# Optimization experiments

Hardware: AMD Instinct MI355X
Metric: run time of the kernel (lower is better)

## Reference

```python
import jax, jax.numpy as jnp
import numpy as np

B, T, C = 4, 2048, 1024
H, D = 16, 64  # num_heads, head_dim
WINDOW = 256


def setup_inputs() -> dict:
    key = jax.random.key(0)
    k_x, k_qkv, k_proj, k_qb, k_pb = jax.random.split(key, 5)
    x = jax.random.normal(k_x, (B, T, C), dtype=jnp.float32)
    # xavier-uniform-ish init for qkv weight (as in _reset_parameters)
    lim_qkv = float(np.sqrt(6.0 / (C + 3 * C)))
    qkv_w = jax.random.uniform(k_qkv, (3 * C, C), minval=-lim_qkv, maxval=lim_qkv, dtype=jnp.float32)
    qkv_b = jax.random.normal(k_qb, (3 * C,), dtype=jnp.float32) * 0.02
    lim_p = float(np.sqrt(1.0 / C))
    proj_w = jax.random.uniform(k_proj, (C, C), minval=-lim_p, maxval=lim_p, dtype=jnp.float32)
    proj_b = jax.random.normal(k_pb, (C,), dtype=jnp.float32) * 0.02
    # windowed causal mask: attend to j iff j <= i and i - j < WINDOW
    i = jnp.arange(T)[:, None]
    j = jnp.arange(T)[None, :]
    attn_mask = (j <= i) & (i - j < WINDOW)  # [T, T] bool
    return {"x": x, "attn_mask": attn_mask, "qkv_w": qkv_w, "qkv_b": qkv_b,
            "proj_w": proj_w, "proj_b": proj_b}


def reference(x, attn_mask, qkv_w, qkv_b, proj_w, proj_b):
    qkv = (x @ qkv_w.T + qkv_b).reshape(B, T, 3, H, D)
    qkv = jnp.transpose(qkv, (2, 0, 3, 1, 4))
    q, k, v = qkv[0], qkv[1], qkv[2]
    scale = 1.0 / jnp.sqrt(jnp.asarray(D, dtype=q.dtype))
    scores = jnp.einsum('bhqd,bhkd->bhqk', q, k) * scale  # [B,H,T,T]
    neg = jnp.asarray(jnp.finfo(scores.dtype).min, dtype=scores.dtype)
    scores = jnp.where(attn_mask[None, None], scores, neg)
    attn = jax.nn.softmax(scores, axis=-1)
    out = jnp.einsum('bhqk,bhkd->bhqd', attn, v)  # [B,H,T,D]
    out = jnp.transpose(out, (0, 2, 1, 3)).reshape(B, T, C)
    out = out @ proj_w.T + proj_b
    return out
```

## Files before the change

kernel.cpp:

```cpp
#include <hip/hip_runtime.h>

#define BB 4
#define TT 2048
#define CC 1024
#define HH 16
#define DD 64
#define WIN 256

typedef __attribute__((ext_vector_type(8))) short short8;
typedef __attribute__((ext_vector_type(4))) float floatx4;
typedef unsigned short u16;

__device__ __forceinline__ float bf2f(u16 u) {
    union { unsigned int i; float f; } v; v.i = ((unsigned int)u) << 16; return v.f;
}
__device__ __forceinline__ u16 f2bf(float f) {
    union { float f; unsigned int i; } v; v.f = f;
    unsigned int x = v.i;
    x += ((x >> 16) & 1u) + 0x7FFFu;
    return (u16)(x >> 16);
}

__global__ void cvt_f32_bf16(const float* __restrict__ in, u16* __restrict__ out, int n) {
    int i = (blockIdx.x * 256 + threadIdx.x) * 8;
    if (i >= n) return;
    float4 a = *(const float4*)(in + i);
    float4 b = *(const float4*)(in + i + 4);
    u16 o[8] = { f2bf(a.x), f2bf(a.y), f2bf(a.z), f2bf(a.w),
                 f2bf(b.x), f2bf(b.y), f2bf(b.z), f2bf(b.w) };
    *(uint4*)(out + i) = *(const uint4*)o;
}

__global__ __launch_bounds__(256) void gemm_qkv(
    const u16* __restrict__ A, const u16* __restrict__ Bw,
    const float* __restrict__ bias,
    u16* __restrict__ Qb, u16* __restrict__ Kb, u16* __restrict__ Vb)
{
    const int K = CC;
    __shared__ u16 As[128][40];
    __shared__ u16 Bs[128][40];
    const int tid = threadIdx.x;
    const int wave = tid >> 6, lane = tid & 63;
    const int wm = wave >> 1, wn = wave & 1;
    const int quad = lane >> 4, l15 = lane & 15;
    const int bN = blockIdx.x * 128, bM = blockIdx.y * 128;

    floatx4 acc[4][4] = {};

    for (int k0 = 0; k0 < K; k0 += 32) {
        __syncthreads();
#pragma unroll
        for (int it = 0; it < 2; ++it) {
            int slot = tid + it * 256;
            int r = slot >> 2;
            int c8 = (slot & 3) << 3;
            *(uint4*)&As[r][c8] = *(const uint4*)&A[(size_t)(bM + r) * K + k0 + c8];
            *(uint4*)&Bs[r][c8] = *(const uint4*)&Bw[(size_t)(bN + r) * K + k0 + c8];
        }
        __syncthreads();
        short8 af[4], bf[4];
#pragma unroll
        for (int i = 0; i < 4; ++i) {
            af[i] = *(const short8*)&As[wm * 64 + i * 16 + l15][quad * 8];
            bf[i] = *(const short8*)&Bs[wn * 64 + i * 16 + l15][quad * 8];
        }
#pragma unroll
        for (int mi = 0; mi < 4; ++mi)
#pragma unroll
            for (int ni = 0; ni < 4; ++ni)
                acc[mi][ni] = __builtin_amdgcn_mfma_f32_16x16x32_bf16(af[mi], bf[ni], acc[mi][ni], 0, 0, 0);
    }

#pragma unroll
    for (int mi = 0; mi < 4; ++mi)
#pragma unroll
        for (int ni = 0; ni < 4; ++ni) {
            int col = bN + wn * 64 + ni * 16 + l15;
            float bv = bias[col];
            int which = col >> 10, rem = col & 1023;
            int h = rem >> 6, d = rem & 63;
            u16* dst = which == 0 ? Qb : (which == 1 ? Kb : Vb);
#pragma unroll
            for (int rg = 0; rg < 4; ++rg) {
                int row = bM + wm * 64 + mi * 16 + quad * 4 + rg;
                int b = row >> 11, t = row & 2047;
                float v = acc[mi][ni][rg] + bv;
                dst[(((size_t)(b * HH + h)) * TT + t) * DD + d] = f2bf(v);
            }
        }
}

__global__ __launch_bounds__(256) void gemm_proj(
    const u16* __restrict__ A, const u16* __restrict__ Bw,
    const float* __restrict__ bias, float* __restrict__ Out)
{
    const int K = CC;
    __shared__ u16 As[128][40];
    __shared__ u16 Bs[128][40];
    const int tid = threadIdx.x;
    const int wave = tid >> 6, lane = tid & 63;
    const int wm = wave >> 1, wn = wave & 1;
    const int quad = lane >> 4, l15 = lane & 15;
    const int bN = blockIdx.x * 128, bM = blockIdx.y * 128;

    floatx4 acc[4][4] = {};

    for (int k0 = 0; k0 < K; k0 += 32) {
        __syncthreads();
#pragma unroll
        for (int it = 0; it < 2; ++it) {
            int slot = tid + it * 256;
            int r = slot >> 2;
            int c8 = (slot & 3) << 3;
            *(uint4*)&As[r][c8] = *(const uint4*)&A[(size_t)(bM + r) * K + k0 + c8];
            *(uint4*)&Bs[r][c8] = *(const uint4*)&Bw[(size_t)(bN + r) * K + k0 + c8];
        }
        __syncthreads();
        short8 af[4], bf[4];
#pragma unroll
        for (int i = 0; i < 4; ++i) {
            af[i] = *(const short8*)&As[wm * 64 + i * 16 + l15][quad * 8];
            bf[i] = *(const short8*)&Bs[wn * 64 + i * 16 + l15][quad * 8];
        }
#pragma unroll
        for (int mi = 0; mi < 4; ++mi)
#pragma unroll
            for (int ni = 0; ni < 4; ++ni)
                acc[mi][ni] = __builtin_amdgcn_mfma_f32_16x16x32_bf16(af[mi], bf[ni], acc[mi][ni], 0, 0, 0);
    }

#pragma unroll
    for (int mi = 0; mi < 4; ++mi)
#pragma unroll
        for (int ni = 0; ni < 4; ++ni) {
            int col = bN + wn * 64 + ni * 16 + l15;
            float bv = bias[col];
#pragma unroll
            for (int rg = 0; rg < 4; ++rg) {
                int row = bM + wm * 64 + mi * 16 + quad * 4 + rg;
                Out[(size_t)row * CC + col] = acc[mi][ni][rg] + bv;
            }
        }
}

__global__ __launch_bounds__(256) void attn_mfma(
    const u16* __restrict__ Qb, const u16* __restrict__ Kb, const u16* __restrict__ Vb,
    u16* __restrict__ Y)
{
    __shared__ u16 Ks[64][72];
    __shared__ u16 Vt[64][72];
    __shared__ u16 Ps[4][16][72];

    const int tid = threadIdx.x;
    const int wave = tid >> 6, lane = tid & 63;
    const int quad = lane >> 4, l15 = lane & 15;
    const int q0 = blockIdx.x * 64;
    const int bh = blockIdx.y;
    const int b = bh >> 4, h = bh & 15;
    const u16* Qp = Qb + (size_t)bh * TT * DD;
    const u16* Kp = Kb + (size_t)bh * TT * DD;
    const u16* Vp = Vb + (size_t)bh * TT * DD;
    const int qw = q0 + wave * 16;

    short8 qf[2];
    qf[0] = *(const short8*)&Qp[(size_t)(qw + l15) * DD + quad * 8];
    qf[1] = *(const short8*)&Qp[(size_t)(qw + l15) * DD + 32 + quad * 8];

    float m_i[4] = { -1e30f, -1e30f, -1e30f, -1e30f };
    float l_i[4] = { 0.f, 0.f, 0.f, 0.f };
    floatx4 Oacc[4] = {};

    const int kb = (q0 >= WIN) ? (q0 - WIN) : 0;
    for (int j0 = kb; j0 < q0 + 64; j0 += 64) {
        __syncthreads();
#pragma unroll
        for (int it = 0; it < 2; ++it) {
            int slot = tid + it * 256;
            int j = slot >> 3, c8 = (slot & 7) << 3;
            *(uint4*)&Ks[j][c8] = *(const uint4*)&Kp[(size_t)(j0 + j) * DD + c8];
        }
#pragma unroll
        for (int it = 0; it < 2; ++it) {
            int slot = tid + it * 256;
            int j = slot >> 3, d0 = (slot & 7) << 3;
            uint4 raw = *(const uint4*)&Vp[(size_t)(j0 + j) * DD + d0];
            const u16* u = (const u16*)&raw;
#pragma unroll
            for (int i = 0; i < 8; ++i) {
                int d = d0 + i;
                int col = (((j >> 3) ^ (d >> 3)) << 3) + (j & 7);
                Vt[d][col] = u[i];
            }
        }
        __syncthreads();

        floatx4 Sacc[4] = {};
#pragma unroll
        for (int nt = 0; nt < 4; ++nt) {
            short8 kf0 = *(const short8*)&Ks[nt * 16 + l15][quad * 8];
            short8 kf1 = *(const short8*)&Ks[nt * 16 + l15][32 + quad * 8];
            Sacc[nt] = __builtin_amdgcn_mfma_f32_16x16x32_bf16(qf[0], kf0, Sacc[nt], 0, 0, 0);
            Sacc[nt] = __builtin_amdgcn_mfma_f32_16x16x32_bf16(qf[1], kf1, Sacc[nt], 0, 0, 0);
        }

        float mc[4] = { -1e30f, -1e30f, -1e30f, -1e30f };
#pragma unroll
        for (int nt = 0; nt < 4; ++nt)
#pragma unroll
            for (int r = 0; r < 4; ++r) {
                int q = qw + quad * 4 + r;
                int j = j0 + nt * 16 + l15;
                float s = (j <= q && (q - j) < WIN) ? Sacc[nt][r] * 0.125f : -1e30f;
                Sacc[nt][r] = s;
                mc[r] = fmaxf(mc[r], s);
            }
#pragma unroll
        for (int m = 1; m < 16; m <<= 1)
#pragma unroll
            for (int r = 0; r < 4; ++r) mc[r] = fmaxf(mc[r], __shfl_xor(mc[r], m, 64));

        float alpha[4];
#pragma unroll
        for (int r = 0; r < 4; ++r) {
            float mn = fmaxf(m_i[r], mc[r]);
            alpha[r] = __expf(m_i[r] - mn);
            m_i[r] = mn;
        }
        float rs[4] = { 0.f, 0.f, 0.f, 0.f };
#pragma unroll
        for (int nt = 0; nt < 4; ++nt)
#pragma unroll
            for (int r = 0; r < 4; ++r) {
                float s = Sacc[nt][r];
                float p = (s > -1e29f) ? __expf(s - m_i[r]) : 0.f;
                Sacc[nt][r] = p;
                rs[r] += p;
            }
#pragma unroll
        for (int m = 1; m < 16; m <<= 1)
#pragma unroll
            for (int r = 0; r < 4; ++r) rs[r] += __shfl_xor(rs[r], m, 64);
#pragma unroll
        for (int r = 0; r < 4; ++r) l_i[r] = l_i[r] * alpha[r] + rs[r];
#pragma unroll
        for (int dt = 0; dt < 4; ++dt)
#pragma unroll
            for (int r = 0; r < 4; ++r) Oacc[dt][r] *= alpha[r];

#pragma unroll
        for (int nt = 0; nt < 4; ++nt)
#pragma unroll
            for (int r = 0; r < 4; ++r)
                Ps[wave][quad * 4 + r][nt * 16 + l15] = f2bf(Sacc[nt][r]);

#pragma unroll
        for (int ks = 0; ks < 2; ++ks) {
            short8 pf = *(const short8*)&Ps[wave][l15][ks * 32 + quad * 8];
#pragma unroll
            for (int dt = 0; dt < 4; ++dt) {
                int d = dt * 16 + l15;
                int col = (((ks * 4 + quad) ^ (d >> 3)) << 3);
                short8 vf = *(const short8*)&Vt[d][col];
                Oacc[dt] = __builtin_amdgcn_mfma_f32_16x16x32_bf16(pf, vf, Oacc[dt], 0, 0, 0);
            }
        }
    }

    float inv[4];
#pragma unroll
    for (int r = 0; r < 4; ++r) inv[r] = 1.f / l_i[r];
#pragma unroll
    for (int dt = 0; dt < 4; ++dt)
#pragma unroll
        for (int r = 0; r < 4; ++r) {
            int t = qw + quad * 4 + r;
            int d = dt * 16 + l15;
            Y[((size_t)b * TT + t) * CC + h * DD + d] = f2bf(Oacc[dt][r] * inv[r]);
        }
}

extern "C" void kernel_launch(void* const* d_in, const int* in_sizes, int n_in,
                              void* d_out, int out_size, void* d_ws, size_t ws_size,
                              hipStream_t stream) {
    const float* x      = (const float*)d_in[0];
    const float* qkv_w  = (const float*)d_in[2];
    const float* qkv_b  = (const float*)d_in[3];
    const float* proj_w = (const float*)d_in[4];
    const float* proj_b = (const float*)d_in[5];
    float* out = (float*)d_out;

    u16* xb  = (u16*)d_ws;
    u16* wb  = xb  + (size_t)8192 * 1024;
    u16* pwb = wb  + (size_t)3072 * 1024;
    u16* Qb  = pwb + (size_t)1024 * 1024;
    u16* Kb  = Qb  + (size_t)64 * 2048 * 64;
    u16* Vb  = Kb  + (size_t)64 * 2048 * 64;
    u16* Yb  = Vb  + (size_t)64 * 2048 * 64;

    cvt_f32_bf16<<<4096, 256, 0, stream>>>(x, xb, 8192 * 1024);
    cvt_f32_bf16<<<1536, 256, 0, stream>>>(qkv_w, wb, 3072 * 1024);
    cvt_f32_bf16<<<512, 256, 0, stream>>>(proj_w, pwb, 1024 * 1024);

    gemm_qkv<<<dim3(24, 64), 256, 0, stream>>>(xb, wb, qkv_b, Qb, Kb, Vb);
    attn_mfma<<<dim3(TT / 64, BB * HH), 256, 0, stream>>>(Qb, Kb, Vb, Yb);
    gemm_proj<<<dim3(8, 64), 256, 0, stream>>>(Yb, pwb, proj_b, out);
}
```

Before: 273.4 us.

## Use direct global-to-LDS loads with XOR swizzle in GEMMs; merge conversion kernels

Both GEMM kernels now stage tiles with global_load_lds, which writes global data straight into LDS without passing through registers. LDS uses an unpadded layout with an XOR-swizzled chunk order on write and read to avoid bank conflicts. The three fp32-to-bf16 conversion launches become one kernel that picks its source by block index, cutting launch overhead. The main loop is still single-buffered with two barriers per step, and correctness depends on the swizzle matching the per-wave LDS write order of the direct-load instruction.

```diff
diff --git a/kernel.cpp b/kernel.cpp
--- a/kernel.cpp
+++ b/kernel.cpp
@@ -11,6 +11,13 @@
 typedef __attribute__((ext_vector_type(4))) float floatx4;
 typedef unsigned short u16;
 
+typedef __attribute__((address_space(3))) void lds_void;
+typedef const __attribute__((address_space(1))) void g_void;
+
+__device__ __forceinline__ void gl_lds16(const u16* g, u16* l) {
+    __builtin_amdgcn_global_load_lds((g_void*)g, (lds_void*)l, 16, 0, 0);
+}
+
 __device__ __forceinline__ float bf2f(u16 u) {
     union { unsigned int i; float f; } v; v.i = ((unsigned int)u) << 16; return v.f;
 }
@@ -21,15 +28,22 @@
     return (u16)(x >> 16);
 }
 
-__global__ void cvt_f32_bf16(const float* __restrict__ in, u16* __restrict__ out, int n) {
-    int i = (blockIdx.x * 256 + threadIdx.x) * 8;
-    if (i >= n) return;
-    float4 a = *(const float4*)(in + i);
-    float4 b = *(const float4*)(in + i + 4);
+__global__ void cvt_all(const float* __restrict__ x, const float* __restrict__ qw,
+                        const float* __restrict__ pw,
+                        u16* __restrict__ xb, u16* __restrict__ wb, u16* __restrict__ pwb) {
+    int bid = blockIdx.x;
+    const float* src; u16* dst; int off;
+    if (bid < 4096)      { src = x;  dst = xb;  off = bid; }
+    else if (bid < 5632) { src = qw; dst = wb;  off = bid - 4096; }
+    else                 { src = pw; dst = pwb; off = bid - 5632; }
+    int i = (off * 256 + (int)threadIdx.x) * 8;
+    float4 a = *(const float4*)(src + i);
+    float4 b = *(const float4*)(src + i + 4);
     u16 o[8] = { f2bf(a.x), f2bf(a.y), f2bf(a.z), f2bf(a.w),
                  f2bf(b.x), f2bf(b.y), f2bf(b.z), f2bf(b.w) };
-    *(uint4*)(out + i) = *(const uint4*)o;
-}
+    *(uint4*)(dst + i) = *(const uint4*)o;
+}
+
 
 __global__ __launch_bounds__(256) void gemm_qkv(
     const u16* __restrict__ A, const u16* __restrict__ Bw,
@@ -37,32 +51,42 @@
     u16* __restrict__ Qb, u16* __restrict__ Kb, u16* __restrict__ Vb)
 {
     const int K = CC;
-    __shared__ u16 As[128][40];
-    __shared__ u16 Bs[128][40];
+    __shared__ u16 As[4096];
+    __shared__ u16 Bs[4096];
     const int tid = threadIdx.x;
     const int wave = tid >> 6, lane = tid & 63;
     const int wm = wave >> 1, wn = wave & 1;
     const int quad = lane >> 4, l15 = lane & 15;
     const int bN = blockIdx.x * 128, bM = blockIdx.y * 128;
 
+    const int srow0 = wave * 16 + (lane >> 2);
+    const int srow1 = (wave + 4) * 16 + (lane >> 2);
+    const int schunk = ((lane & 3) ^ ((lane >> 3) & 3)) * 8;
+    const u16* gA0 = A + (size_t)(bM + srow0) * K + schunk;
+    const u16* gA1 = A + (size_t)(bM + srow1) * K + schunk;
+    const u16* gB0 = Bw + (size_t)(bN + srow0) * K + schunk;
+    const u16* gB1 = Bw + (size_t)(bN + srow1) * K + schunk;
+    u16* lA0 = &As[wave * 512];
+    u16* lA1 = &As[(wave + 4) * 512];
+    u16* lB0 = &Bs[wave * 512];
+    u16* lB1 = &Bs[(wave + 4) * 512];
+
+    const int rdoff = l15 * 32 + ((quad ^ ((l15 >> 1) & 3)) * 8);
+
     floatx4 acc[4][4] = {};
 
     for (int k0 = 0; k0 < K; k0 += 32) {
         __syncthreads();
-#pragma unroll
-        for (int it = 0; it < 2; ++it) {
-            int slot = tid + it * 256;
-            int r = slot >> 2;
-            int c8 = (slot & 3) << 3;
-            *(uint4*)&As[r][c8] = *(const uint4*)&A[(size_t)(bM + r) * K + k0 + c8];
-            *(uint4*)&Bs[r][c8] = *(const uint4*)&Bw[(size_t)(bN + r) * K + k0 + c8];
-        }
+        gl_lds16(gA0 + k0, lA0);
+        gl_lds16(gA1 + k0, lA1);
+        gl_lds16(gB0 + k0, lB0);
+        gl_lds16(gB1 + k0, lB1);
         __syncthreads();
         short8 af[4], bf[4];
 #pragma unroll
         for (int i = 0; i < 4; ++i) {
-            af[i] = *(const short8*)&As[wm * 64 + i * 16 + l15][quad * 8];
-            bf[i] = *(const short8*)&Bs[wn * 64 + i * 16 + l15][quad * 8];
+            af[i] = *(const short8*)&As[(wm * 4 + i) * 512 + rdoff];
+            bf[i] = *(const short8*)&Bs[(wn * 4 + i) * 512 + rdoff];
         }
 #pragma unroll
         for (int mi = 0; mi < 4; ++mi)
@@ -95,32 +119,42 @@
     const float* __restrict__ bias, float* __restrict__ Out)
 {
     const int K = CC;
-    __shared__ u16 As[128][40];
-    __shared__ u16 Bs[128][40];
+    __shared__ u16 As[4096];
+    __shared__ u16 Bs[4096];
     const int tid = threadIdx.x;
     const int wave = tid >> 6, lane = tid & 63;
     const int wm = wave >> 1, wn = wave & 1;
     const int quad = lane >> 4, l15 = lane & 15;
     const int bN = blockIdx.x * 128, bM = blockIdx.y * 128;
 
+    const int srow0 = wave * 16 + (lane >> 2);
+    const int srow1 = (wave + 4) * 16 + (lane >> 2);
+    const int schunk = ((lane & 3) ^ ((lane >> 3) & 3)) * 8;
+    const u16* gA0 = A + (size_t)(bM + srow0) * K + schunk;
+    const u16* gA1 = A + (size_t)(bM + srow1) * K + schunk;
+    const u16* gB0 = Bw + (size_t)(bN + srow0) * K + schunk;
+    const u16* gB1 = Bw + (size_t)(bN + srow1) * K + schunk;
+    u16* lA0 = &As[wave * 512];
+    u16* lA1 = &As[(wave + 4) * 512];
+    u16* lB0 = &Bs[wave * 512];
+    u16* lB1 = &Bs[(wave + 4) * 512];
+
+    const int rdoff = l15 * 32 + ((quad ^ ((l15 >> 1) & 3)) * 8);
+
     floatx4 acc[4][4] = {};
 
     for (int k0 = 0; k0 < K; k0 += 32) {
         __syncthreads();
-#pragma unroll
-        for (int it = 0; it < 2; ++it) {
-            int slot = tid + it * 256;
-            int r = slot >> 2;
-            int c8 = (slot & 3) << 3;
-            *(uint4*)&As[r][c8] = *(const uint4*)&A[(size_t)(bM + r) * K + k0 + c8];
-            *(uint4*)&Bs[r][c8] = *(const uint4*)&Bw[(size_t)(bN + r) * K + k0 + c8];
-        }
+        gl_lds16(gA0 + k0, lA0);
+        gl_lds16(gA1 + k0, lA1);
+        gl_lds16(gB0 + k0, lB0);
+        gl_lds16(gB1 + k0, lB1);
         __syncthreads();
         short8 af[4], bf[4];
 #pragma unroll
         for (int i = 0; i < 4; ++i) {
-            af[i] = *(const short8*)&As[wm * 64 + i * 16 + l15][quad * 8];
-            bf[i] = *(const short8*)&Bs[wn * 64 + i * 16 + l15][quad * 8];
+            af[i] = *(const short8*)&As[(wm * 4 + i) * 512 + rdoff];
+            bf[i] = *(const short8*)&Bs[(wn * 4 + i) * 512 + rdoff];
         }
 #pragma unroll
         for (int mi = 0; mi < 4; ++mi)
@@ -297,10 +331,7 @@
     u16* Vb  = Kb  + (size_t)64 * 2048 * 64;
     u16* Yb  = Vb  + (size_t)64 * 2048 * 64;
 
-    cvt_f32_bf16<<<4096, 256, 0, stream>>>(x, xb, 8192 * 1024);
-    cvt_f32_bf16<<<1536, 256, 0, stream>>>(qkv_w, wb, 3072 * 1024);
-    cvt_f32_bf16<<<512, 256, 0, stream>>>(proj_w, pwb, 1024 * 1024);
-
+    cvt_all<<<6144, 256, 0, stream>>>(x, qkv_w, proj_w, xb, wb, pwb);
     gemm_qkv<<<dim3(24, 64), 256, 0, stream>>>(xb, wb, qkv_b, Qb, Kb, Vb);
     attn_mfma<<<dim3(TT / 64, BB * HH), 256, 0, stream>>>(Qb, Kb, Vb, Yb);
     gemm_proj<<<dim3(8, 64), 256, 0, stream>>>(Yb, pwb, proj_b, out);
```

New measurement: 238.3 us. 1.15x faster.
